# Kernel tuning notes

Hardware: AMD Instinct MI355X
Metric: run time of the kernel (lower is better)

The kernel has to match this reference:

```python
import jax, jax.numpy as jnp
import numpy as np

N = 50000
E = 500000
C = 128
NUM_TYPES = 32
DIM_TOK = 94
STEPS = 3
BLOCKS = 2
NUM_ET = 3
LN_EPS = 1e-5


def setup_inputs() -> dict:
    key = jax.random.key(0)
    ks = jax.random.split(key, 16)
    s = 0.05
    return {
        "x_type": jax.random.randint(ks[0], (N,), 0, NUM_TYPES),
        "x_tok": jax.random.randint(ks[1], (N,), 0, DIM_TOK),
        "x_small": jax.random.normal(ks[2], (N, 2), jnp.float32),
        "edge_index": jax.random.randint(ks[3], (2, E), 0, N),
        "edge_type": jax.random.randint(ks[4], (E,), 0, NUM_ET),
        "conv_w": jax.random.normal(ks[5], (BLOCKS, NUM_ET, STEPS, C, C), jnp.float32) * s,
        "gru_wih": jax.random.normal(ks[6], (BLOCKS, NUM_ET, 3 * C, C), jnp.float32) * s,
        "gru_whh": jax.random.normal(ks[7], (BLOCKS, NUM_ET, 3 * C, C), jnp.float32) * s,
        "gru_bih": jnp.zeros((BLOCKS, NUM_ET, 3 * C), jnp.float32),
        "gru_bhh": jnp.zeros((BLOCKS, NUM_ET, 3 * C), jnp.float32),
        "ln_g": jnp.ones((BLOCKS, C), jnp.float32),
        "ln_b": jnp.zeros((BLOCKS, C), jnp.float32),
        "head_w1": jax.random.normal(ks[8], (C, C), jnp.float32) * s,
        "head_b1": jnp.zeros((C,), jnp.float32),
        "head_w2": jax.random.normal(ks[9], (2, C), jnp.float32) * s,
        "head_b2": jnp.zeros((2,), jnp.float32),
    }


def _gru_cell(x, h, wih, whh, bih, bhh):
    # torch.nn.GRUCell: gates ordered (r, z, n)
    gi = x @ wih.T + bih  # [N, 3C]
    gh = h @ whh.T + bhh
    gi_r, gi_z, gi_n = jnp.split(gi, 3, axis=-1)
    gh_r, gh_z, gh_n = jnp.split(gh, 3, axis=-1)
    r = jax.nn.sigmoid(gi_r + gh_r)
    z = jax.nn.sigmoid(gi_z + gh_z)
    n = jnp.tanh(gi_n + r * gh_n)
    return (1.0 - z) * n + z * h


def _forward(x_small, conv_w, gru_wih, gru_whh, gru_bih, gru_bhh, ln_g, ln_b,
             head_w1, head_b1, head_w2, head_b2, x_type, x_tok, edge_index, edge_type):
    # build_features: one-hot type, one-hot (clamped) token, small feats
    h_type = jax.nn.one_hot(x_type, NUM_TYPES, dtype=x_small.dtype)
    h_tok = jax.nn.one_hot(jnp.clip(x_tok, 0, DIM_TOK - 1), DIM_TOK, dtype=x_small.dtype)
    h = jnp.concatenate([h_type, h_tok, x_small], axis=1)  # [N, C]

    src, dst = edge_index[0], edge_index[1]

    for b in range(BLOCKS):
        total = jnp.zeros_like(h)
        for t in range(NUM_ET):
            # edge-type masking implemented as weighted scatter-add (sum aggr)
            em = (edge_type == t).astype(h.dtype)[:, None]  # [E, 1]
            m = h
            for s in range(STEPS):
                x = m @ conv_w[b, t, s]                     # [N, C]
                agg = jax.ops.segment_sum(x[src] * em, dst, num_segments=N)
                m = _gru_cell(agg, m,
                              gru_wih[b, t], gru_whh[b, t],
                              gru_bih[b, t], gru_bhh[b, t])
            total = total + m
        # LayerNorm(residual) + ReLU; dropout=0 (eval)
        hr = h + total
        mu = jnp.mean(hr, axis=-1, keepdims=True)
        var = jnp.var(hr, axis=-1, keepdims=True)
        h = (hr - mu) * jax.lax.rsqrt(var + LN_EPS) * ln_g[b] + ln_b[b]
        h = jax.nn.relu(h)

    # head applied per-node (module returns head(h), not head(pooled))
    z = jax.nn.relu(h @ head_w1.T + head_b1)
    return z @ head_w2.T + head_b2  # [N, 2]


def reference(x_type, x_tok, x_small, edge_index, edge_type, conv_w, gru_wih, gru_whh,
              gru_bih, gru_bhh, ln_g, ln_b, head_w1, head_b1, head_w2, head_b2):
    return _forward(x_small, conv_w, gru_wih, gru_whh, gru_bih, gru_bhh, ln_g, ln_b,
                    head_w1, head_b1, head_w2, head_b2, x_type, x_tok, edge_index, edge_type)
```

## Files before the change

### kernel.cpp

```cpp
#include <hip/hip_runtime.h>
#include <cstdint>
#include <cstddef>

#define N_NODES 50000
#define N_EDGES 500000
#define NB 782
#define NT 150000
#define NCHUNK2 586
#define FS 49152
#define PSTR 136
#define MAXOFF 12799744u
#define ECAP 1024

typedef _Float16 half8 __attribute__((ext_vector_type(8)));
typedef _Float16 half2v __attribute__((ext_vector_type(2)));
typedef float floatx4 __attribute__((ext_vector_type(4)));

__device__ __forceinline__ float sigmoid_(float x) { return 1.f / (1.f + __expf(-x)); }
__device__ __forceinline__ float tanh_(float x) {
  float t = __expf(-2.f * fabsf(x));
  float r = (1.f - t) / (1.f + t);
  return copysignf(r, x);
}

__global__ __launch_bounds__(256) void k_features(_Float16* __restrict__ h,
    const int* __restrict__ xtype, const int* __restrict__ xtok,
    const float* __restrict__ xs) {
  int idx = blockIdx.x * 256 + threadIdx.x;
  if (idx >= N_NODES * 128) return;
  int n = idx >> 7, c = idx & 127;
  float v;
  if (c < 32) {
    v = (xtype[n] == c) ? 1.f : 0.f;
  } else if (c < 126) {
    int tk = xtok[n];
    tk = tk < 0 ? 0 : (tk > 93 ? 93 : tk);
    v = (tk == (c - 32)) ? 1.f : 0.f;
  } else {
    v = xs[n * 2 + (c - 126)];
  }
  h[idx] = (_Float16)v;
}

__global__ __launch_bounds__(256) void k_hist(const int* __restrict__ ei,
    const int* __restrict__ et, int* __restrict__ counts) {
  int e = blockIdx.x * 256 + threadIdx.x;
  if (e >= N_EDGES) return;
  int d = ei[N_EDGES + e];
  int ty = et[e] & 3;
  if ((unsigned)d < N_NODES && ty < 3) atomicAdd(&counts[ty * N_NODES + d], 1);
}

__global__ __launch_bounds__(256) void k_scan_a(const int* __restrict__ counts,
    int* __restrict__ bsum) {
  int i = blockIdx.x * 256 + threadIdx.x;
  int v = (i < NT) ? counts[i] : 0;
  int lane = threadIdx.x & 63, wv = threadIdx.x >> 6;
#pragma unroll
  for (int off = 32; off > 0; off >>= 1) v += __shfl_xor(v, off);
  __shared__ int ws[4];
  if (lane == 0) ws[wv] = v;
  __syncthreads();
  if (threadIdx.x == 0) bsum[blockIdx.x] = ws[0] + ws[1] + ws[2] + ws[3];
}

__global__ __launch_bounds__(256) void k_scan_b(const int* __restrict__ bsum,
    int* __restrict__ boff) {
  __shared__ int ws[4];
  __shared__ int run_s;
  if (threadIdx.x == 0) run_s = 0;
  __syncthreads();
  int lane = threadIdx.x & 63, wv = threadIdx.x >> 6;
  for (int base = 0; base < NCHUNK2; base += 256) {
    int i = base + threadIdx.x;
    int v = (i < NCHUNK2) ? bsum[i] : 0;
    int s = v;
#pragma unroll
    for (int off = 1; off < 64; off <<= 1) { int u = __shfl_up(s, off); if (lane >= off) s += u; }
    if (lane == 63) ws[wv] = s;
    __syncthreads();
    int woff = 0;
#pragma unroll
    for (int w = 0; w < 4; ++w) woff += (w < wv) ? ws[w] : 0;
    int run = run_s;
    if (i < NCHUNK2) boff[i] = run + woff + s - v;
    __syncthreads();
    if (threadIdx.x == 255) run_s = run + woff + s;
    __syncthreads();
  }
  if (threadIdx.x == 0) boff[NCHUNK2] = run_s;
}

__global__ __launch_bounds__(256) void k_scan_c(const int* __restrict__ counts,
    const int* __restrict__ boff, int* __restrict__ ptr, int* __restrict__ fill) {
  int i = blockIdx.x * 256 + threadIdx.x;
  int v = (i < NT) ? counts[i] : 0;
  int lane = threadIdx.x & 63, wv = threadIdx.x >> 6;
  int s = v;
#pragma unroll
  for (int off = 1; off < 64; off <<= 1) { int u = __shfl_up(s, off); if (lane >= off) s += u; }
  __shared__ int ws[4];
  if (lane == 63) ws[wv] = s;
  __syncthreads();
  int woff = 0;
#pragma unroll
  for (int w = 0; w < 4; ++w) woff += (w < wv) ? ws[w] : 0;
  int excl = boff[blockIdx.x] + woff + s - v;
  if (i < NT) { ptr[i] = excl; fill[i] = excl; }
  if (blockIdx.x == 0 && threadIdx.x == 0) ptr[NT] = boff[NCHUNK2];
}

__global__ __launch_bounds__(256) void k_place(const int* __restrict__ ei,
    const int* __restrict__ et, int* __restrict__ fill, int* __restrict__ csr) {
  int e = blockIdx.x * 256 + threadIdx.x;
  if (e >= N_EDGES) return;
  int srcv = ei[e], d = ei[N_EDGES + e], ty = et[e] & 3;
  if ((unsigned)d >= N_NODES || (unsigned)srcv >= N_NODES || ty >= 3) return;
  int pos = atomicAdd(&fill[ty * N_NODES + d], 1);
  if ((unsigned)pos < N_EDGES) csr[pos] = srcv << 8;
}


__global__ __launch_bounds__(512) void k_prep_cmb(const float* __restrict__ cw,
    const float* __restrict__ wih, _Float16* __restrict__ dst) {
  int mat = blockIdx.x >> 1, half = blockIdx.x & 1;
  int bt = mat / 3;
  int u = threadIdx.x >> 6, lane = threadIdx.x & 63;
  int quad = lane >> 4, l16 = lane & 15;
  floatx4 zero = {0.f, 0.f, 0.f, 0.f};
  floatx4 acc[4][3];
#pragma unroll
  for (int rt = 0; rt < 4; ++rt)
#pragma unroll
    for (int cc = 0; cc < 3; ++cc) acc[rt][cc] = zero;
#pragma unroll
  for (int jc = 0; jc < 4; ++jc) {
    half8 af[4], bf[3];
#pragma unroll
    for (int rt = 0; rt < 4; ++rt) {
      int m = half * 64 + rt * 16 + l16;
      const float* ap = cw + ((size_t)mat * 128 + m) * 128 + jc * 32 + quad * 8;
      floatx4 a0 = *(const floatx4*)ap;
      floatx4 a1 = *(const floatx4*)(ap + 4);
#pragma unroll
      for (int i = 0; i < 4; ++i) { af[rt][i] = (_Float16)a0[i]; af[rt][4 + i] = (_Float16)a1[i]; }
    }
#pragma unroll
    for (int cc = 0; cc < 3; ++cc) {
      int n = (u * 3 + cc) * 16 + l16;
      const float* bp = wih + ((size_t)bt * 384 + n) * 128 + jc * 32 + quad * 8;
      floatx4 b0 = *(const floatx4*)bp;
      floatx4 b1 = *(const floatx4*)(bp + 4);
#pragma unroll
      for (int i = 0; i < 4; ++i) { bf[cc][i] = (_Float16)b0[i]; bf[cc][4 + i] = (_Float16)b1[i]; }
    }
#pragma unroll
    for (int rt = 0; rt < 4; ++rt)
#pragma unroll
      for (int cc = 0; cc < 3; ++cc)
        acc[rt][cc] = __builtin_amdgcn_mfma_f32_16x16x32_f16(af[rt], bf[cc], acc[rt][cc], 0, 0, 0);
  }
#pragma unroll
  for (int rt = 0; rt < 4; ++rt) {
#pragma unroll
    for (int cc = 0; cc < 3; ++cc) {
      int ctg = u * 3 + cc;
#pragma unroll
      for (int q = 0; q < 4; ++q) {
        int k = half * 64 + rt * 16 + quad * 4 + q;
        int kc2 = k >> 5, r5 = k & 31;
        int lane2 = (r5 >> 3) * 16 + l16, j2 = r5 & 7;
        dst[(size_t)mat * FS + (size_t)((kc2 * 24 + ctg) * 64 + lane2) * 8 + j2] =
            (_Float16)acc[rt][cc][q];
      }
    }
  }
}

#define PREP_B (6 * 4 * 24 * 512)
__global__ __launch_bounds__(256) void k_prep_misc(const float* __restrict__ whh,
    const float* __restrict__ hw1, _Float16* __restrict__ dwhh,
    _Float16* __restrict__ dw1) {
  int idx0 = blockIdx.x * 256 + threadIdx.x;
  if (idx0 < PREP_B) {
    int idx = idx0;
    int j = idx & 7, lane = (idx >> 3) & 63;
    int r = idx >> 9;
    int ct = r % 24;
    int r2 = r / 24;
    int kc = r2 & 3, bt = r2 >> 2;
    int k = kc * 32 + ((lane >> 4) & 3) * 8 + j;
    int n = ct * 16 + (lane & 15);
    dwhh[idx] = (_Float16)whh[((size_t)bt * 384 + n) * 128 + k];
  } else if (idx0 < PREP_B + 16384) {
    int idx = idx0 - PREP_B;
    int j = idx & 7, lane = (idx >> 3) & 63, ct = (idx >> 9) & 7, kc = (idx >> 12) & 3;
    int k = kc * 32 + ((lane >> 4) & 3) * 8 + j;
    int n = ct * 16 + (lane & 15);
    dw1[idx] = (_Float16)hw1[n * 128 + k];
  }
}

__global__ __launch_bounds__(512, 4) void k_step(
    const _Float16* __restrict__ Mbase, const size_t mstride,
    _Float16* __restrict__ Sout,
    const int* __restrict__ ptr, const int* __restrict__ csr,
    const _Float16* __restrict__ WPC, const _Float16* __restrict__ WHH,
    const float* __restrict__ bi2, const float* __restrict__ bh2) {
  __shared__ __attribute__((aligned(16))) _Float16 Plds[64 * PSTR];
  __shared__ __attribute__((aligned(16))) _Float16 Mlds[64 * PSTR];
  __shared__ int Elds[ECAP];
  __shared__ int Pt[65];
  int bid = blockIdx.x;
  int t = bid / NB, blk = bid - t * NB;
  int tid = threadIdx.x;
  int wave = tid >> 6, lane = tid & 63;
  int quad = lane >> 4, l16 = lane & 15;
  int rowbase = blk * 64;
  const size_t NC = (size_t)N_NODES * 128;
  const _Float16* Mp = Mbase + mstride * t;
  const char* Mb = (const char*)Mp;
  _Float16* Sp = Sout + (size_t)t * NC;
  const int* ptrT = ptr + t * N_NODES;

  int rb64 = rowbase + 64; if (rb64 > N_NODES) rb64 = N_NODES;
  int bse = ptrT[rowbase];
  int cend = ptrT[rb64];
  if (bse < 0) bse = 0; if (bse > N_EDGES) bse = N_EDGES;
  if (cend < bse) cend = bse; if (cend > N_EDGES) cend = N_EDGES;
  int cnt = cend - bse; if (cnt > ECAP) cnt = ECAP;

  if (tid < 65) {
    int n = rowbase + tid; if (n > N_NODES) n = N_NODES;
    int v = ptrT[n] - bse;
    if (v < 0) v = 0; if (v > cnt) v = cnt;
    Pt[tid] = v;
  }
#pragma unroll
  for (int it = 0; it < 2; ++it) {
    int r = it * 32 + (tid >> 4);
    int c = (tid & 15) * 8;
    int gr = rowbase + r; if (gr >= N_NODES) gr = N_NODES - 1;
    half8 v = *(const half8*)(Mp + (size_t)gr * 128 + c);
    *(half8*)(&Mlds[r * PSTR + c]) = v;
  }
  for (int i = tid; i < cnt; i += 512) {
    unsigned off = (unsigned)csr[bse + i];
    if (off > MAXOFF) off = 0;
    Elds[i] = (int)off;
  }
  __syncthreads();

  int g = quad;
  unsigned coff = (unsigned)(l16 * 16);
  int nlA = wave * 8 + g, nlB = nlA + 4;
  int iA = Pt[nlA], eA = Pt[nlA + 1];
  int iB = Pt[nlB], eB = Pt[nlB + 1];
  half8 accA = {}, accB = {};
  while (__any(iA < eA || iB < eB)) {
#pragma unroll
    for (int uu = 0; uu < 4; ++uu) {
      if (iA + uu < eA) {
        unsigned o = (unsigned)Elds[iA + uu] + coff;
        accA += *(const half8*)(Mb + o);
      }
      if (iB + uu < eB) {
        unsigned o = (unsigned)Elds[iB + uu] + coff;
        accB += *(const half8*)(Mb + o);
      }
    }
    iA += 4; iB += 4;
  }
  *(half8*)(&Plds[nlA * PSTR + l16 * 8]) = accA;
  *(half8*)(&Plds[nlB * PSTR + l16 * 8]) = accB;
  __syncthreads();

  const half8* wpc = (const half8*)(WPC + (size_t)t * 3 * FS);
  const half8* whh = (const half8*)(WHH + (size_t)t * FS);
  const float* bi = bi2 + (size_t)t * 384;
  const float* bh = bh2 + (size_t)t * 384;
  int u = wave;
  floatx4 zero = {0.f, 0.f, 0.f, 0.f};
  floatx4 aR[4], aZ[4], aNP[4], aNM[4];
#pragma unroll
  for (int rt = 0; rt < 4; ++rt) { aR[rt] = zero; aZ[rt] = zero; aNP[rt] = zero; aNM[rt] = zero; }
#pragma unroll
  for (int kc = 0; kc < 4; ++kc) {
    half8 af[4];
#pragma unroll
    for (int rt = 0; rt < 4; ++rt)
      af[rt] = *(const half8*)(&Plds[(rt * 16 + l16) * PSTR + kc * 32 + quad * 8]);
    half8 br = wpc[(kc * 24 + u) * 64 + lane];
    half8 bz = wpc[(kc * 24 + 8 + u) * 64 + lane];
    half8 bn = wpc[(kc * 24 + 16 + u) * 64 + lane];
#pragma unroll
    for (int rt = 0; rt < 4; ++rt) {
      aR[rt] = __builtin_amdgcn_mfma_f32_16x16x32_f16(af[rt], br, aR[rt], 0, 0, 0);
      aZ[rt] = __builtin_amdgcn_mfma_f32_16x16x32_f16(af[rt], bz, aZ[rt], 0, 0, 0);
      aNP[rt] = __builtin_amdgcn_mfma_f32_16x16x32_f16(af[rt], bn, aNP[rt], 0, 0, 0);
    }
  }
#pragma unroll
  for (int kc = 0; kc < 4; ++kc) {
    half8 af[4];
#pragma unroll
    for (int rt = 0; rt < 4; ++rt)
      af[rt] = *(const half8*)(&Mlds[(rt * 16 + l16) * PSTR + kc * 32 + quad * 8]);
    half8 br = whh[(kc * 24 + u) * 64 + lane];
    half8 bz = whh[(kc * 24 + 8 + u) * 64 + lane];
    half8 bn = whh[(kc * 24 + 16 + u) * 64 + lane];
#pragma unroll
    for (int rt = 0; rt < 4; ++rt) {
      aR[rt] = __builtin_amdgcn_mfma_f32_16x16x32_f16(af[rt], br, aR[rt], 0, 0, 0);
      aZ[rt] = __builtin_amdgcn_mfma_f32_16x16x32_f16(af[rt], bz, aZ[rt], 0, 0, 0);
      aNM[rt] = __builtin_amdgcn_mfma_f32_16x16x32_f16(af[rt], bn, aNM[rt], 0, 0, 0);
    }
  }
  __syncthreads();
  int col = u * 16 + l16;
  float br_ = bi[col] + bh[col];
  float bz_ = bi[128 + col] + bh[128 + col];
  float bin = bi[256 + col], bhn = bh[256 + col];
#pragma unroll
  for (int rt = 0; rt < 4; ++rt) {
#pragma unroll
    for (int q = 0; q < 4; ++q) {
      int lr = rt * 16 + quad * 4 + q;
      float r = sigmoid_(aR[rt][q] + br_);
      float z = sigmoid_(aZ[rt][q] + bz_);
      float nt = tanh_(aNP[rt][q] + bin + r * (aNM[rt][q] + bhn));
      float hold = (float)Mlds[lr * PSTR + col];
      Plds[lr * PSTR + col] = (_Float16)((1.f - z) * nt + z * hold);
    }
  }
  __syncthreads();
#pragma unroll
  for (int it = 0; it < 2; ++it) {
    int r = it * 32 + (tid >> 4);
    int c = (tid & 15) * 8;
    int row = rowbase + r;
    if (row < N_NODES)
      *(half8*)(Sp + (size_t)row * 128 + c) = *(const half8*)(&Plds[r * PSTR + c]);
  }
}

__global__ __launch_bounds__(256) void k_ln(_Float16* __restrict__ h,
    const _Float16* __restrict__ S, const float* __restrict__ gamma,
    const float* __restrict__ beta) {
  int wave = threadIdx.x >> 6, lane = threadIdx.x & 63;
  int n = blockIdx.x * 4 + wave;
  if (n >= N_NODES) return;
  const size_t NC = (size_t)N_NODES * 128;
  size_t base = (size_t)n * 128 + lane * 2;
  half2v hv = *(const half2v*)(h + base);
  half2v s0 = *(const half2v*)(S + base);
  half2v s1 = *(const half2v*)(S + NC + base);
  half2v s2 = *(const half2v*)(S + 2 * NC + base);
  float v0 = (float)hv[0] + (float)s0[0] + (float)s1[0] + (float)s2[0];
  float v1 = (float)hv[1] + (float)s0[1] + (float)s1[1] + (float)s2[1];
  float s = v0 + v1, sq = v0 * v0 + v1 * v1;
#pragma unroll
  for (int off = 32; off > 0; off >>= 1) {
    s += __shfl_xor(s, off);
    sq += __shfl_xor(sq, off);
  }
  float mu = s * 0.0078125f;
  float var = sq * 0.0078125f - mu * mu;
  float rs = rsqrtf(var + 1e-5f);
  float o0 = (v0 - mu) * rs * gamma[lane * 2] + beta[lane * 2];
  float o1 = (v1 - mu) * rs * gamma[lane * 2 + 1] + beta[lane * 2 + 1];
  half2v ov; ov[0] = (_Float16)fmaxf(o0, 0.f); ov[1] = (_Float16)fmaxf(o1, 0.f);
  *(half2v*)(h + base) = ov;
}

__global__ __launch_bounds__(256, 4) void k_head(const _Float16* __restrict__ A,
    const _Float16* __restrict__ Wf, const float* __restrict__ bias,
    const float* __restrict__ w2, const float* __restrict__ b2,
    float* __restrict__ out) {
  __shared__ __attribute__((aligned(16))) _Float16 zl[64 * PSTR];
  __shared__ float w2s[256];
  int blk = blockIdx.x;
  int wave = threadIdx.x >> 6, lane = threadIdx.x & 63;
  int quad = lane >> 4, l16 = lane & 15;
  int rowbase = blk * 64;
  if (threadIdx.x < 256) w2s[threadIdx.x] = w2[threadIdx.x];
  const half8* wf = (const half8*)Wf;
  int ar[4];
#pragma unroll
  for (int rt = 0; rt < 4; ++rt) {
    int r = rowbase + rt * 16 + l16;
    ar[rt] = r < N_NODES ? r : N_NODES - 1;
  }
  floatx4 zero = {0.f, 0.f, 0.f, 0.f};
  floatx4 acc[4][2];
#pragma unroll
  for (int rt = 0; rt < 4; ++rt) { acc[rt][0] = zero; acc[rt][1] = zero; }
#pragma unroll
  for (int kc = 0; kc < 4; ++kc) {
    half8 af[4];
#pragma unroll
    for (int rt = 0; rt < 4; ++rt)
      af[rt] = *(const half8*)(A + (size_t)ar[rt] * 128 + kc * 32 + quad * 8);
    half8 b0 = wf[(kc * 8 + 2 * wave) * 64 + lane];
    half8 b1 = wf[(kc * 8 + 2 * wave + 1) * 64 + lane];
#pragma unroll
    for (int rt = 0; rt < 4; ++rt) {
      acc[rt][0] = __builtin_amdgcn_mfma_f32_16x16x32_f16(af[rt], b0, acc[rt][0], 0, 0, 0);
      acc[rt][1] = __builtin_amdgcn_mfma_f32_16x16x32_f16(af[rt], b1, acc[rt][1], 0, 0, 0);
    }
  }
  int col = wave * 32 + l16;
#pragma unroll
  for (int rt = 0; rt < 4; ++rt) {
#pragma unroll
    for (int q = 0; q < 4; ++q) {
      int lr = rt * 16 + quad * 4 + q;
      zl[lr * PSTR + col] = (_Float16)fmaxf(acc[rt][0][q] + bias[col], 0.f);
      zl[lr * PSTR + col + 16] = (_Float16)fmaxf(acc[rt][1][q] + bias[col + 16], 0.f);
    }
  }
  __syncthreads();
  int tid = threadIdx.x;
  if (tid < 128) {
    int lr = tid >> 1, o = tid & 1;
    int row = rowbase + lr;
    if (row < N_NODES) {
      const float* wr = w2s + o * 128;
      float a = 0.f;
#pragma unroll
      for (int k = 0; k < 128; ++k) a += (float)zl[lr * PSTR + k] * wr[k];
      out[(size_t)row * 2 + o] = a + b2[o];
    }
  }
}

extern "C" void kernel_launch(void* const* d_in, const int* in_sizes, int n_in,
                              void* d_out, int out_size, void* d_ws, size_t ws_size,
                              hipStream_t stream) {
  const int*   x_type  = (const int*)d_in[0];
  const int*   x_tok   = (const int*)d_in[1];
  const float* x_small = (const float*)d_in[2];
  const int*   eidx    = (const int*)d_in[3];
  const int*   etype   = (const int*)d_in[4];
  const float* conv_w  = (const float*)d_in[5];
  const float* gwih    = (const float*)d_in[6];
  const float* gwhh    = (const float*)d_in[7];
  const float* gbih    = (const float*)d_in[8];
  const float* gbhh    = (const float*)d_in[9];
  const float* ln_g    = (const float*)d_in[10];
  const float* ln_b    = (const float*)d_in[11];
  const float* hw1     = (const float*)d_in[12];
  const float* hb1     = (const float*)d_in[13];
  const float* hw2     = (const float*)d_in[14];
  const float* hb2     = (const float*)d_in[15];
  float* out = (float*)d_out;

  const size_t NC = (size_t)N_NODES * 128;
  char* W = (char*)d_ws;
  size_t off = 0;
  _Float16* h16 = (_Float16*)(W + off);     off += NC * 2;
  _Float16* S0  = (_Float16*)(W + off);     off += 3 * NC * 2;
  _Float16* S1  = (_Float16*)(W + off);     off += 3 * NC * 2;
  int* counts = (int*)(W + off);            off += (size_t)NT * 4;
  int* ptrv   = (int*)(W + off);            off += (size_t)(NT + 1) * 4;
  int* fill   = (int*)(W + off);            off += (size_t)NT * 4;
  int* bsum   = (int*)(W + off);            off += (NCHUNK2 + 1) * 4;
  int* boff   = (int*)(W + off);            off += (NCHUNK2 + 1) * 4;
  int* csr    = (int*)(W + off);            off += (size_t)N_EDGES * 4;
  _Float16* WPC = (_Float16*)(W + off);     off += (size_t)18 * FS * 2;
  _Float16* WHH = (_Float16*)(W + off);     off += (size_t)6 * FS * 2;
  _Float16* W1F = (_Float16*)(W + off);     off += (size_t)16384 * 2;

  k_features<<<(N_NODES * 128 + 255) / 256, 256, 0, stream>>>(h16, x_type, x_tok, x_small);
  hipMemsetAsync(counts, 0, (size_t)NT * 4, stream);
  k_hist<<<(N_EDGES + 255) / 256, 256, 0, stream>>>(eidx, etype, counts);
  k_scan_a<<<NCHUNK2, 256, 0, stream>>>(counts, bsum);
  k_scan_b<<<1, 256, 0, stream>>>(bsum, boff);
  k_scan_c<<<NCHUNK2, 256, 0, stream>>>(counts, boff, ptrv, fill);
  k_place<<<(N_EDGES + 255) / 256, 256, 0, stream>>>(eidx, etype, fill, csr);
  k_prep_cmb<<<36, 512, 0, stream>>>(conv_w, gwih, WPC);
  k_prep_misc<<<(PREP_B + 16384 + 255) / 256, 256, 0, stream>>>(gwhh, hw1, WHH, W1F);

  for (int b = 0; b < 2; ++b) {
    for (int s = 0; s < 3; ++s) {
      const _Float16* Msrc = (s == 0) ? h16 : ((s == 1) ? S0 : S1);
      size_t mstr = (s == 0) ? 0 : NC;
      _Float16* Sout = (s == 1) ? S1 : S0;
      k_step<<<3 * NB, 512, 0, stream>>>(Msrc, mstr, Sout, ptrv, csr,
          WPC + (size_t)(b * 9 + s) * FS, WHH + (size_t)b * 3 * FS,
          gbih + (size_t)b * 3 * 384, gbhh + (size_t)b * 3 * 384);
    }
    k_ln<<<(N_NODES + 3) / 4, 256, 0, stream>>>(h16, S0, ln_g + b * 128, ln_b + b * 128);
  }
  k_head<<<NB, 256, 0, stream>>>(h16, W1F, hb1, hw2, hb2, out);
}
```

Measured before the change: 681.7 us.

## Fuse setup kernels, drop scan pass, fuse final LayerNorm into head

Merges feature build with edge histogram, merges the two weight prep kernels, and removes the single-block scan by having each scan block sum preceding block totals itself. Vectorizes LayerNorm to 8 halves per lane and fuses the last block's LayerNorm into the head kernel through shared memory. Also replaces the __any-driven gather loop in k_step with a precomputed trip count. These cut launch count and intermediate traffic. The trade-off is redundant bsum reads in the scan and extra shared memory in the head kernel.

Result: no change. 670.6 us (-1.6%).

```diff
diff --git a/kernel.cpp b/kernel.cpp
--- a/kernel.cpp
+++ b/kernel.cpp
@@ -23,32 +23,30 @@
   return copysignf(r, x);
 }
 
-__global__ __launch_bounds__(256) void k_features(_Float16* __restrict__ h,
+__global__ __launch_bounds__(256) void k_feat_hist(_Float16* __restrict__ h,
     const int* __restrict__ xtype, const int* __restrict__ xtok,
-    const float* __restrict__ xs) {
+    const float* __restrict__ xs, const int* __restrict__ ei,
+    const int* __restrict__ et, int* __restrict__ counts) {
   int idx = blockIdx.x * 256 + threadIdx.x;
-  if (idx >= N_NODES * 128) return;
-  int n = idx >> 7, c = idx & 127;
-  float v;
-  if (c < 32) {
-    v = (xtype[n] == c) ? 1.f : 0.f;
-  } else if (c < 126) {
-    int tk = xtok[n];
-    tk = tk < 0 ? 0 : (tk > 93 ? 93 : tk);
-    v = (tk == (c - 32)) ? 1.f : 0.f;
-  } else {
-    v = xs[n * 2 + (c - 126)];
-  }
-  h[idx] = (_Float16)v;
-}
-
-__global__ __launch_bounds__(256) void k_hist(const int* __restrict__ ei,
-    const int* __restrict__ et, int* __restrict__ counts) {
-  int e = blockIdx.x * 256 + threadIdx.x;
-  if (e >= N_EDGES) return;
-  int d = ei[N_EDGES + e];
-  int ty = et[e] & 3;
-  if ((unsigned)d < N_NODES && ty < 3) atomicAdd(&counts[ty * N_NODES + d], 1);
+  if (idx < N_NODES * 128) {
+    int n = idx >> 7, c = idx & 127;
+    float v;
+    if (c < 32) {
+      v = (xtype[n] == c) ? 1.f : 0.f;
+    } else if (c < 126) {
+      int tk = xtok[n];
+      tk = tk < 0 ? 0 : (tk > 93 ? 93 : tk);
+      v = (tk == (c - 32)) ? 1.f : 0.f;
+    } else {
+      v = xs[n * 2 + (c - 126)];
+    }
+    h[idx] = (_Float16)v;
+  }
+  if (idx < N_EDGES) {
+    int d = ei[N_EDGES + idx];
+    int ty = et[idx] & 3;
+    if ((unsigned)d < N_NODES && ty < 3) atomicAdd(&counts[ty * N_NODES + d], 1);
+  }
 }
 
 __global__ __launch_bounds__(256) void k_scan_a(const int* __restrict__ counts,
@@ -64,50 +62,32 @@
   if (threadIdx.x == 0) bsum[blockIdx.x] = ws[0] + ws[1] + ws[2] + ws[3];
 }
 
-__global__ __launch_bounds__(256) void k_scan_b(const int* __restrict__ bsum,
-    int* __restrict__ boff) {
+__global__ __launch_bounds__(256) void k_scan_c(const int* __restrict__ counts,
+    const int* __restrict__ bsum, int* __restrict__ ptr, int* __restrict__ fill) {
+  __shared__ int wsum2[4];
   __shared__ int ws[4];
-  __shared__ int run_s;
-  if (threadIdx.x == 0) run_s = 0;
-  __syncthreads();
   int lane = threadIdx.x & 63, wv = threadIdx.x >> 6;
-  for (int base = 0; base < NCHUNK2; base += 256) {
-    int i = base + threadIdx.x;
-    int v = (i < NCHUNK2) ? bsum[i] : 0;
-    int s = v;
-#pragma unroll
-    for (int off = 1; off < 64; off <<= 1) { int u = __shfl_up(s, off); if (lane >= off) s += u; }
-    if (lane == 63) ws[wv] = s;
-    __syncthreads();
-    int woff = 0;
-#pragma unroll
-    for (int w = 0; w < 4; ++w) woff += (w < wv) ? ws[w] : 0;
-    int run = run_s;
-    if (i < NCHUNK2) boff[i] = run + woff + s - v;
-    __syncthreads();
-    if (threadIdx.x == 255) run_s = run + woff + s;
-    __syncthreads();
-  }
-  if (threadIdx.x == 0) boff[NCHUNK2] = run_s;
-}
-
-__global__ __launch_bounds__(256) void k_scan_c(const int* __restrict__ counts,
-    const int* __restrict__ boff, int* __restrict__ ptr, int* __restrict__ fill) {
+  int acc = 0;
+  for (int j = threadIdx.x; j < blockIdx.x; j += 256) acc += bsum[j];
+#pragma unroll
+  for (int off = 32; off > 0; off >>= 1) acc += __shfl_xor(acc, off);
+  if (lane == 0) wsum2[wv] = acc;
+  __syncthreads();
+  int boffset = wsum2[0] + wsum2[1] + wsum2[2] + wsum2[3];
   int i = blockIdx.x * 256 + threadIdx.x;
   int v = (i < NT) ? counts[i] : 0;
-  int lane = threadIdx.x & 63, wv = threadIdx.x >> 6;
   int s = v;
 #pragma unroll
   for (int off = 1; off < 64; off <<= 1) { int u = __shfl_up(s, off); if (lane >= off) s += u; }
-  __shared__ int ws[4];
   if (lane == 63) ws[wv] = s;
   __syncthreads();
   int woff = 0;
 #pragma unroll
   for (int w = 0; w < 4; ++w) woff += (w < wv) ? ws[w] : 0;
-  int excl = boff[blockIdx.x] + woff + s - v;
+  int excl = boffset + woff + s - v;
   if (i < NT) { ptr[i] = excl; fill[i] = excl; }
-  if (blockIdx.x == 0 && threadIdx.x == 0) ptr[NT] = boff[NCHUNK2];
+  if (blockIdx.x == NCHUNK2 - 1 && threadIdx.x == 0)
+    ptr[NT] = boffset + bsum[NCHUNK2 - 1];
 }
 
 __global__ __launch_bounds__(256) void k_place(const int* __restrict__ ei,
@@ -120,84 +100,84 @@
   if ((unsigned)pos < N_EDGES) csr[pos] = srcv << 8;
 }
 
-
-__global__ __launch_bounds__(512) void k_prep_cmb(const float* __restrict__ cw,
-    const float* __restrict__ wih, _Float16* __restrict__ dst) {
-  int mat = blockIdx.x >> 1, half = blockIdx.x & 1;
-  int bt = mat / 3;
-  int u = threadIdx.x >> 6, lane = threadIdx.x & 63;
-  int quad = lane >> 4, l16 = lane & 15;
-  floatx4 zero = {0.f, 0.f, 0.f, 0.f};
-  floatx4 acc[4][3];
-#pragma unroll
-  for (int rt = 0; rt < 4; ++rt)
-#pragma unroll
-    for (int cc = 0; cc < 3; ++cc) acc[rt][cc] = zero;
-#pragma unroll
-  for (int jc = 0; jc < 4; ++jc) {
-    half8 af[4], bf[3];
+#define PREP_B (6 * 4 * 24 * 512)
+#define PREP_MISC_BLOCKS ((PREP_B + 16384 + 511) / 512)
+__global__ __launch_bounds__(512) void k_prep(const float* __restrict__ cw,
+    const float* __restrict__ wih, const float* __restrict__ whh,
+    const float* __restrict__ hw1, _Float16* __restrict__ dcomb,
+    _Float16* __restrict__ dwhh, _Float16* __restrict__ dw1) {
+  if (blockIdx.x < 36) {
+    int mat = blockIdx.x >> 1, half = blockIdx.x & 1;
+    int bt = mat / 3;
+    int u = threadIdx.x >> 6, lane = threadIdx.x & 63;
+    int quad = lane >> 4, l16 = lane & 15;
+    floatx4 zero = {0.f, 0.f, 0.f, 0.f};
+    floatx4 acc[4][3];
+#pragma unroll
+    for (int rt = 0; rt < 4; ++rt)
+#pragma unroll
+      for (int cc = 0; cc < 3; ++cc) acc[rt][cc] = zero;
+#pragma unroll
+    for (int jc = 0; jc < 4; ++jc) {
+      half8 af[4], bf[3];
+#pragma unroll
+      for (int rt = 0; rt < 4; ++rt) {
+        int m = half * 64 + rt * 16 + l16;
+        const float* ap = cw + ((size_t)mat * 128 + m) * 128 + jc * 32 + quad * 8;
+        floatx4 a0 = *(const floatx4*)ap;
+        floatx4 a1 = *(const floatx4*)(ap + 4);
+#pragma unroll
+        for (int i = 0; i < 4; ++i) { af[rt][i] = (_Float16)a0[i]; af[rt][4 + i] = (_Float16)a1[i]; }
+      }
+#pragma unroll
+      for (int cc = 0; cc < 3; ++cc) {
+        int n = (u * 3 + cc) * 16 + l16;
+        const float* bp = wih + ((size_t)bt * 384 + n) * 128 + jc * 32 + quad * 8;
+        floatx4 b0 = *(const floatx4*)bp;
+        floatx4 b1 = *(const floatx4*)(bp + 4);
+#pragma unroll
+        for (int i = 0; i < 4; ++i) { bf[cc][i] = (_Float16)b0[i]; bf[cc][4 + i] = (_Float16)b1[i]; }
+      }
+#pragma unroll
+      for (int rt = 0; rt < 4; ++rt)
+#pragma unroll
+        for (int cc = 0; cc < 3; ++cc)
+          acc[rt][cc] = __builtin_amdgcn_mfma_f32_16x16x32_f16(af[rt], bf[cc], acc[rt][cc], 0, 0, 0);
+    }
 #pragma unroll
     for (int rt = 0; rt < 4; ++rt) {
-      int m = half * 64 + rt * 16 + l16;
-      const float* ap = cw + ((size_t)mat * 128 + m) * 128 + jc * 32 + quad * 8;
-      floatx4 a0 = *(const floatx4*)ap;
-      floatx4 a1 = *(const floatx4*)(ap + 4);
-#pragma unroll
-      for (int i = 0; i < 4; ++i) { af[rt][i] = (_Float16)a0[i]; af[rt][4 + i] = (_Float16)a1[i]; }
-    }
-#pragma unroll
-    for (int cc = 0; cc < 3; ++cc) {
-      int n = (u * 3 + cc) * 16 + l16;
-      const float* bp = wih + ((size_t)bt * 384 + n) * 128 + jc * 32 + quad * 8;
-      floatx4 b0 = *(const floatx4*)bp;
-      floatx4 b1 = *(const floatx4*)(bp + 4);
-#pragma unroll
-      for (int i = 0; i < 4; ++i) { bf[cc][i] = (_Float16)b0[i]; bf[cc][4 + i] = (_Float16)b1[i]; }
-    }
-#pragma unroll
-    for (int rt = 0; rt < 4; ++rt)
-#pragma unroll
-      for (int cc = 0; cc < 3; ++cc)
-        acc[rt][cc] = __builtin_amdgcn_mfma_f32_16x16x32_f16(af[rt], bf[cc], acc[rt][cc], 0, 0, 0);
-  }
-#pragma unroll
-  for (int rt = 0; rt < 4; ++rt) {
-#pragma unroll
-    for (int cc = 0; cc < 3; ++cc) {
-      int ctg = u * 3 + cc;
-#pragma unroll
-      for (int q = 0; q < 4; ++q) {
-        int k = half * 64 + rt * 16 + quad * 4 + q;
-        int kc2 = k >> 5, r5 = k & 31;
-        int lane2 = (r5 >> 3) * 16 + l16, j2 = r5 & 7;
-        dst[(size_t)mat * FS + (size_t)((kc2 * 24 + ctg) * 64 + lane2) * 8 + j2] =
-            (_Float16)acc[rt][cc][q];
+#pragma unroll
+      for (int cc = 0; cc < 3; ++cc) {
+        int ctg = u * 3 + cc;
+#pragma unroll
+        for (int q = 0; q < 4; ++q) {
+          int k = half * 64 + rt * 16 + quad * 4 + q;
+          int kc2 = k >> 5, r5 = k & 31;
+          int lane2 = (r5 >> 3) * 16 + l16, j2 = r5 & 7;
+          dcomb[(size_t)mat * FS + (size_t)((kc2 * 24 + ctg) * 64 + lane2) * 8 + j2] =
+              (_Float16)acc[rt][cc][q];
+        }
       }
     }
-  }
-}
-
-#define PREP_B (6 * 4 * 24 * 512)
-__global__ __launch_bounds__(256) void k_prep_misc(const float* __restrict__ whh,
-    const float* __restrict__ hw1, _Float16* __restrict__ dwhh,
-    _Float16* __restrict__ dw1) {
-  int idx0 = blockIdx.x * 256 + threadIdx.x;
-  if (idx0 < PREP_B) {
-    int idx = idx0;
-    int j = idx & 7, lane = (idx >> 3) & 63;
-    int r = idx >> 9;
-    int ct = r % 24;
-    int r2 = r / 24;
-    int kc = r2 & 3, bt = r2 >> 2;
-    int k = kc * 32 + ((lane >> 4) & 3) * 8 + j;
-    int n = ct * 16 + (lane & 15);
-    dwhh[idx] = (_Float16)whh[((size_t)bt * 384 + n) * 128 + k];
-  } else if (idx0 < PREP_B + 16384) {
-    int idx = idx0 - PREP_B;
-    int j = idx & 7, lane = (idx >> 3) & 63, ct = (idx >> 9) & 7, kc = (idx >> 12) & 3;
-    int k = kc * 32 + ((lane >> 4) & 3) * 8 + j;
-    int n = ct * 16 + (lane & 15);
-    dw1[idx] = (_Float16)hw1[n * 128 + k];
+  } else {
+    int idx0 = (blockIdx.x - 36) * 512 + threadIdx.x;
+    if (idx0 < PREP_B) {
+      int idx = idx0;
+      int j = idx & 7, lane = (idx >> 3) & 63;
+      int r = idx >> 9;
+      int ct = r % 24;
+      int r2 = r / 24;
+      int kc = r2 & 3, bt = r2 >> 2;
+      int k = kc * 32 + ((lane >> 4) & 3) * 8 + j;
+      int n = ct * 16 + (lane & 15);
+      dwhh[idx] = (_Float16)whh[((size_t)bt * 384 + n) * 128 + k];
+    } else if (idx0 < PREP_B + 16384) {
+      int idx = idx0 - PREP_B;
+      int j = idx & 7, lane = (idx >> 3) & 63, ct = (idx >> 9) & 7, kc = (idx >> 12) & 3;
+      int k = kc * 32 + ((lane >> 4) & 3) * 8 + j;
+      int n = ct * 16 + (lane & 15);
+      dw1[idx] = (_Float16)hw1[n * 128 + k];
+    }
   }
 }
 
@@ -256,8 +236,13 @@
   int nlA = wave * 8 + g, nlB = nlA + 4;
   int iA = Pt[nlA], eA = Pt[nlA + 1];
   int iB = Pt[nlB], eB = Pt[nlB + 1];
+  int need = eA - iA;
+  int nb = eB - iB; if (nb > need) need = nb;
+  int m1 = __shfl_xor(need, 16); if (m1 > need) need = m1;
+  int m2 = __shfl_xor(need, 32); if (m2 > need) need = m2;
+  int trips = (need + 3) >> 2;
   half8 accA = {}, accB = {};
-  while (__any(iA < eA || iB < eB)) {
+  for (int it = 0; it < trips; ++it) {
 #pragma unroll
     for (int uu = 0; uu < 4; ++uu) {
       if (iA + uu < eA) {
@@ -344,53 +329,90 @@
   }
 }
 
-__global__ __launch_bounds__(256) void k_ln(_Float16* __restrict__ h,
+__global__ __launch_bounds__(256) void k_ln16(_Float16* __restrict__ h,
     const _Float16* __restrict__ S, const float* __restrict__ gamma,
     const float* __restrict__ beta) {
   int wave = threadIdx.x >> 6, lane = threadIdx.x & 63;
-  int n = blockIdx.x * 4 + wave;
-  if (n >= N_NODES) return;
+  int g = lane >> 4, l16 = lane & 15;
+  int row = blockIdx.x * 16 + wave * 4 + g;
+  if (row >= N_NODES) return;
   const size_t NC = (size_t)N_NODES * 128;
-  size_t base = (size_t)n * 128 + lane * 2;
-  half2v hv = *(const half2v*)(h + base);
-  half2v s0 = *(const half2v*)(S + base);
-  half2v s1 = *(const half2v*)(S + NC + base);
-  half2v s2 = *(const half2v*)(S + 2 * NC + base);
-  float v0 = (float)hv[0] + (float)s0[0] + (float)s1[0] + (float)s2[0];
-  float v1 = (float)hv[1] + (float)s0[1] + (float)s1[1] + (float)s2[1];
-  float s = v0 + v1, sq = v0 * v0 + v1 * v1;
-#pragma unroll
-  for (int off = 32; off > 0; off >>= 1) {
+  size_t base = (size_t)row * 128 + l16 * 8;
+  half8 hv = *(const half8*)(h + base);
+  half8 s0 = *(const half8*)(S + base);
+  half8 s1 = *(const half8*)(S + NC + base);
+  half8 s2 = *(const half8*)(S + 2 * NC + base);
+  float v[8];
+  float s = 0.f, sq = 0.f;
+#pragma unroll
+  for (int i = 0; i < 8; ++i) {
+    v[i] = (float)hv[i] + (float)s0[i] + (float)s1[i] + (float)s2[i];
+    s += v[i]; sq += v[i] * v[i];
+  }
+#pragma unroll
+  for (int off = 1; off < 16; off <<= 1) {
     s += __shfl_xor(s, off);
     sq += __shfl_xor(sq, off);
   }
   float mu = s * 0.0078125f;
   float var = sq * 0.0078125f - mu * mu;
   float rs = rsqrtf(var + 1e-5f);
-  float o0 = (v0 - mu) * rs * gamma[lane * 2] + beta[lane * 2];
-  float o1 = (v1 - mu) * rs * gamma[lane * 2 + 1] + beta[lane * 2 + 1];
-  half2v ov; ov[0] = (_Float16)fmaxf(o0, 0.f); ov[1] = (_Float16)fmaxf(o1, 0.f);
-  *(half2v*)(h + base) = ov;
-}
-
-__global__ __launch_bounds__(256, 4) void k_head(const _Float16* __restrict__ A,
-    const _Float16* __restrict__ Wf, const float* __restrict__ bias,
-    const float* __restrict__ w2, const float* __restrict__ b2,
-    float* __restrict__ out) {
-  __shared__ __attribute__((aligned(16))) _Float16 zl[64 * PSTR];
+  half8 ov;
+#pragma unroll
+  for (int i = 0; i < 8; ++i) {
+    float o = (v[i] - mu) * rs * gamma[l16 * 8 + i] + beta[l16 * 8 + i];
+    ov[i] = (_Float16)fmaxf(o, 0.f);
+  }
+  *(half8*)(h + base) = ov;
+}
+
+__global__ __launch_bounds__(256, 4) void k_head(const _Float16* __restrict__ h,
+    const _Float16* __restrict__ S, const float* __restrict__ gamma,
+    const float* __restrict__ beta, const _Float16* __restrict__ Wf,
+    const float* __restrict__ bias, const float* __restrict__ w2,
+    const float* __restrict__ b2, float* __restrict__ out) {
+  __shared__ __attribute__((aligned(16))) _Float16 zA[64 * PSTR];
+  __shared__ __attribute__((aligned(16))) _Float16 zB[64 * PSTR];
   __shared__ float w2s[256];
-  int blk = blockIdx.x;
   int wave = threadIdx.x >> 6, lane = threadIdx.x & 63;
   int quad = lane >> 4, l16 = lane & 15;
-  int rowbase = blk * 64;
-  if (threadIdx.x < 256) w2s[threadIdx.x] = w2[threadIdx.x];
+  int rowbase = blockIdx.x * 64;
+  const size_t NC = (size_t)N_NODES * 128;
+  w2s[threadIdx.x] = w2[threadIdx.x];
+#pragma unroll
+  for (int pass = 0; pass < 4; ++pass) {
+    int rl = pass * 16 + wave * 4 + quad;
+    int row = rowbase + rl; if (row >= N_NODES) row = N_NODES - 1;
+    size_t base = (size_t)row * 128 + l16 * 8;
+    half8 hv = *(const half8*)(h + base);
+    half8 s0 = *(const half8*)(S + base);
+    half8 s1 = *(const half8*)(S + NC + base);
+    half8 s2 = *(const half8*)(S + 2 * NC + base);
+    float v[8];
+    float s = 0.f, sq = 0.f;
+#pragma unroll
+    for (int i = 0; i < 8; ++i) {
+      v[i] = (float)hv[i] + (float)s0[i] + (float)s1[i] + (float)s2[i];
+      s += v[i]; sq += v[i] * v[i];
+    }
+#pragma unroll
+    for (int off = 1; off < 16; off <<= 1) {
+      s += __shfl_xor(s, off);
+      sq += __shfl_xor(sq, off);
+    }
+    float mu = s * 0.0078125f;
+    float var = sq * 0.0078125f - mu * mu;
+    float rs = rsqrtf(var + 1e-5f);
+    half8 ov;
+#pragma unroll
+    for (int i = 0; i < 8; ++i) {
+      float o = (v[i] - mu) * rs * gamma[l16 * 8 + i] + beta[l16 * 8 + i];
+      ov[i] = (_Float16)fmaxf(o, 0.f);
+    }
+    *(half8*)(&zA[rl * PSTR + l16 * 8]) = ov;
+  }
+  __syncthreads();
   const half8* wf = (const half8*)Wf;
-  int ar[4];
-#pragma unroll
-  for (int rt = 0; rt < 4; ++rt) {
-    int r = rowbase + rt * 16 + l16;
-    ar[rt] = r < N_NODES ? r : N_NODES - 1;
-  }
   floatx4 zero = {0.f, 0.f, 0.f, 0.f};
   floatx4 acc[4][2];
 #pragma unroll
@@ -400,7 +422,7 @@
     half8 af[4];
 #pragma unroll
     for (int rt = 0; rt < 4; ++rt)
-      af[rt] = *(const half8*)(A + (size_t)ar[rt] * 128 + kc * 32 + quad * 8);
+      af[rt] = *(const half8*)(&zA[(rt * 16 + l16) * PSTR + kc * 32 + quad * 8]);
     half8 b0 = wf[(kc * 8 + 2 * wave) * 64 + lane];
     half8 b1 = wf[(kc * 8 + 2 * wave + 1) * 64 + lane];
 #pragma unroll
@@ -415,8 +437,8 @@
 #pragma unroll
     for (int q = 0; q < 4; ++q) {
       int lr = rt * 16 + quad * 4 + q;
-      zl[lr * PSTR + col] = (_Float16)fmaxf(acc[rt][0][q] + bias[col], 0.f);
-      zl[lr * PSTR + col + 16] = (_Float16)fmaxf(acc[rt][1][q] + bias[col + 16], 0.f);
+      zB[lr * PSTR + col] = (_Float16)fmaxf(acc[rt][0][q] + bias[col], 0.f);
+      zB[lr * PSTR + col + 16] = (_Float16)fmaxf(acc[rt][1][q] + bias[col + 16], 0.f);
     }
   }
   __syncthreads();
@@ -428,7 +450,7 @@
       const float* wr = w2s + o * 128;
       float a = 0.f;
 #pragma unroll
-      for (int k = 0; k < 128; ++k) a += (float)zl[lr * PSTR + k] * wr[k];
+      for (int k = 0; k < 128; ++k) a += (float)zB[lr * PSTR + k] * wr[k];
       out[(size_t)row * 2 + o] = a + b2[o];
     }
   }
@@ -465,21 +487,19 @@
   int* ptrv   = (int*)(W + off);            off += (size_t)(NT + 1) * 4;
   int* fill   = (int*)(W + off);            off += (size_t)NT * 4;
   int* bsum   = (int*)(W + off);            off += (NCHUNK2 + 1) * 4;
-  int* boff   = (int*)(W + off);            off += (NCHUNK2 + 1) * 4;
   int* csr    = (int*)(W + off);            off += (size_t)N_EDGES * 4;
   _Float16* WPC = (_Float16*)(W + off);     off += (size_t)18 * FS * 2;
   _Float16* WHH = (_Float16*)(W + off);     off += (size_t)6 * FS * 2;
   _Float16* W1F = (_Float16*)(W + off);     off += (size_t)16384 * 2;
 
-  k_features<<<(N_NODES * 128 + 255) / 256, 256, 0, stream>>>(h16, x_type, x_tok, x_small);
   hipMemsetAsync(counts, 0, (size_t)NT * 4, stream);
-  k_hist<<<(N_EDGES + 255) / 256, 256, 0, stream>>>(eidx, etype, counts);
+  k_feat_hist<<<(N_NODES * 128 + 255) / 256, 256, 0, stream>>>(
+      h16, x_type, x_tok, x_small, eidx, etype, counts);
   k_scan_a<<<NCHUNK2, 256, 0, stream>>>(counts, bsum);
-  k_scan_b<<<1, 256, 0, stream>>>(bsum, boff);
-  k_scan_c<<<NCHUNK2, 256, 0, stream>>>(counts, boff, ptrv, fill);
+  k_scan_c<<<NCHUNK2, 256, 0, stream>>>(counts, bsum, ptrv, fill);
   k_place<<<(N_EDGES + 255) / 256, 256, 0, stream>>>(eidx, etype, fill, csr);
-  k_prep_cmb<<<36, 512, 0, stream>>>(conv_w, gwih, WPC);
-  k_prep_misc<<<(PREP_B + 16384 + 255) / 256, 256, 0, stream>>>(gwhh, hw1, WHH, W1F);
+  k_prep<<<36 + PREP_MISC_BLOCKS, 512, 0, stream>>>(
+      conv_w, gwih, gwhh, hw1, WPC, WHH, W1F);
 
   for (int b = 0; b < 2; ++b) {
     for (int s = 0; s < 3; ++s) {
@@ -490,7 +510,9 @@
           WPC + (size_t)(b * 9 + s) * FS, WHH + (size_t)b * 3 * FS,
           gbih + (size_t)b * 3 * 384, gbhh + (size_t)b * 3 * 384);
     }
-    k_ln<<<(N_NODES + 3) / 4, 256, 0, stream>>>(h16, S0, ln_g + b * 128, ln_b + b * 128);
-  }
-  k_head<<<NB, 256, 0, stream>>>(h16, W1F, hb1, hw2, hb2, out);
-}
+    if (b == 0)
+      k_ln16<<<(N_NODES + 15) / 16, 256, 0, stream>>>(h16, S0, ln_g, ln_b);
+  }
+  k_head<<<NB, 256, 0, stream>>>(h16, S0, ln_g + 128, ln_b + 128,
+                                 W1F, hb1, hw2, hb2, out);
+}
```
